# Optimization experiments

Measured on AMD Instinct MI355X. Metric: run time of the kernel, lower is better.

## Reference

```python
import jax, jax.numpy as jnp
import numpy as np

B, T, C, H, DH = 2, 2048, 768, 12, 64


def setup_inputs() -> dict:
    key = jax.random.key(0)
    k1, k2, k3 = jax.random.split(key, 3)
    x = jax.random.normal(k1, (B, T, C), dtype=jnp.float32)
    Wqkv = jax.random.normal(k2, (C, 3 * C), dtype=jnp.float32) * (C ** -0.5)
    Wout = jax.random.normal(k3, (C, C), dtype=jnp.float32) * (C ** -0.5)
    return {"x": x, "Wqkv": Wqkv, "Wout": Wout}


def reference(x, Wqkv, Wout):
    b, t, c = x.shape
    qkv = x @ Wqkv  # [B,T,3C]
    q, k, v = jnp.split(qkv, 3, axis=-1)
    # [B,T,C] -> [B,H,T,dh]
    q = q.reshape(b, t, H, DH).transpose(0, 2, 1, 3)
    k = k.reshape(b, t, H, DH).transpose(0, 2, 1, 3)
    v = v.reshape(b, t, H, DH).transpose(0, 2, 1, 3)
    scale = DH ** -0.5
    scores = jnp.einsum('bhqd,bhkd->bhqk', q, k) * scale  # [B,H,T,T]
    causal = jnp.tril(jnp.ones((t, t), dtype=bool))
    scores = jnp.where(causal, scores, -jnp.inf)
    weights = jax.nn.softmax(scores, axis=-1)
    # dropout p=0.0 -> identity
    out = jnp.einsum('bhqk,bhkd->bhqd', weights, v)  # [B,H,T,dh]
    out = out.transpose(0, 2, 1, 3).reshape(b, t, c)
    return out @ Wout
```

## Files before the change

kernel.cpp:

```cpp
#include <hip/hip_runtime.h>
#include <hip/hip_bf16.h>

#define Bn 2
#define Tn 2048
#define Cn 768
#define Hn 12
#define Dn 64
#define N3n 2304
#define Mn 4096

#define MASKVAL (-30000.f)
#define NITEMS 768
#define DEFER_THR 64.f
#define L2E8 0.1803368801111204f

typedef unsigned short u16;
typedef __attribute__((ext_vector_type(8))) unsigned short ushort8_t;
typedef __attribute__((ext_vector_type(8))) short bf16x8;
typedef __attribute__((ext_vector_type(4))) float f32x4;
typedef __attribute__((address_space(1))) unsigned int* gas1_t;
typedef __attribute__((address_space(3))) unsigned int* las3_t;

__device__ __forceinline__ float bf2f(u16 u) {
  union { unsigned int i; float f; } v; v.i = ((unsigned int)u) << 16; return v.f;
}
__device__ __forceinline__ u16 f2bf(float f) {
  union { float f; unsigned int i; } v; v.f = f;
  return (u16)((v.i + 0x7fffu + ((v.i >> 16) & 1u)) >> 16);
}

__global__ __launch_bounds__(256) void cast_bf16(const float* __restrict__ in,
                                                 u16* __restrict__ out,
                                                 int* __restrict__ counter) {
  if (blockIdx.x == 0 && threadIdx.x == 0) *counter = 0;
  const int i = (blockIdx.x * 256 + threadIdx.x) * 4;
  float4 v = *(const float4*)(in + i);
  ushort4 s;
  s.x = f2bf(v.x); s.y = f2bf(v.y); s.z = f2bf(v.z); s.w = f2bf(v.w);
  *(ushort4*)(out + i) = s;
}

__global__ __launch_bounds__(256) void transpose_cast(const float* __restrict__ in,
                                                      u16* __restrict__ out,
                                                      int R, int Cc) {
  __shared__ u16 t[32][33];
  const int c0 = blockIdx.x * 32, r0 = blockIdx.y * 32;
  const int tx = threadIdx.x, ty = threadIdx.y;
#pragma unroll
  for (int i = 0; i < 4; i++)
    t[ty * 4 + i][tx] = f2bf(in[(size_t)(r0 + ty * 4 + i) * Cc + c0 + tx]);
  __syncthreads();
#pragma unroll
  for (int i = 0; i < 4; i++)
    out[(size_t)(c0 + ty * 4 + i) * R + r0 + tx] = t[tx][ty * 4 + i];
}

#define BK 64

template <int EPI>
__global__ __launch_bounds__(256) void mfma_gemm(const u16* __restrict__ A,
                                                 const u16* __restrict__ BT,
                                                 u16* __restrict__ Q,
                                                 u16* __restrict__ Kd,
                                                 u16* __restrict__ VT,
                                                 float* __restrict__ out) {
  __shared__ __align__(16) u16 Ash[128 * BK];
  __shared__ __align__(16) u16 Bsh[128 * BK];
  const int tid = threadIdx.x;
  const int wv = tid >> 6, lane = tid & 63;
  const int lo = lane & 15, quad = lane >> 4;
  const int wm = wv & 1, wn = wv >> 1;

  const int nwg = gridDim.x * gridDim.y;
  const int cpx = nwg >> 3;
  const int lid = blockIdx.y * gridDim.x + blockIdx.x;
  const int swz = (lid & 7) * cpx + (lid >> 3);
  const int n0 = (swz % gridDim.x) * 128;
  const int m0 = (swz / gridDim.x) * 128;

  const int srow = lane >> 3;
  const int scol = (lane & 7) << 3;

  f32x4 acc[4][4];
#pragma unroll
  for (int i = 0; i < 4; i++)
#pragma unroll
    for (int j = 0; j < 4; j++) acc[i][j] = f32x4{0.f, 0.f, 0.f, 0.f};

  for (int k0 = 0; k0 < Cn; k0 += BK) {
    __syncthreads();
#pragma unroll
    for (int c = 0; c < 4; c++) {
      const int rb = (wv << 5) + (c << 3);
      const int gr = rb + srow;
      __builtin_amdgcn_global_load_lds(
          (gas1_t)(A + (size_t)(m0 + gr) * Cn + k0 + scol),
          (las3_t)(&Ash[rb * BK]), 16, 0, 0);
      __builtin_amdgcn_global_load_lds(
          (gas1_t)(BT + (size_t)(n0 + gr) * Cn + k0 + scol),
          (las3_t)(&Bsh[rb * BK]), 16, 0, 0);
    }
    __syncthreads();

    bf16x8 af[4][2], bfr[4][2];
#pragma unroll
    for (int t = 0; t < 4; t++) {
#pragma unroll
      for (int s = 0; s < 2; s++) {
        af[t][s]  = *(const bf16x8*)&Ash[(wm * 64 + t * 16 + lo) * BK + s * 32 + (quad << 3)];
        bfr[t][s] = *(const bf16x8*)&Bsh[(wn * 64 + t * 16 + lo) * BK + s * 32 + (quad << 3)];
      }
    }
#pragma unroll
    for (int mt = 0; mt < 4; mt++)
#pragma unroll
      for (int nt = 0; nt < 4; nt++) {
        acc[mt][nt] = __builtin_amdgcn_mfma_f32_16x16x32_bf16(af[mt][0], bfr[nt][0],
                                                              acc[mt][nt], 0, 0, 0);
        acc[mt][nt] = __builtin_amdgcn_mfma_f32_16x16x32_bf16(af[mt][1], bfr[nt][1],
                                                              acc[mt][nt], 0, 0, 0);
      }
  }

  if (EPI == 0) {
    const int which = n0 / Cn;
    const int h = ((n0 % Cn) >> 6) + wn;
    const int bb = m0 >> 11;
    const int t_base = (m0 & (Tn - 1)) + wm * 64;
    if (which < 2) {
      u16* dst = ((which == 0) ? Q : Kd) + (size_t)(bb * Hn + h) * Tn * Dn;
#pragma unroll
      for (int mt = 0; mt < 4; mt++)
#pragma unroll
        for (int nt = 0; nt < 4; nt++)
#pragma unroll
          for (int r = 0; r < 4; r++) {
            const int t = t_base + mt * 16 + (quad << 2) + r;
            dst[(size_t)t * Dn + nt * 16 + lo] = f2bf(acc[mt][nt][r]);
          }
    } else {
      u16* dst = VT + (size_t)(bb * Hn + h) * Dn * Tn;
#pragma unroll
      for (int mt = 0; mt < 4; mt++)
#pragma unroll
        for (int nt = 0; nt < 4; nt++) {
          const int t = t_base + mt * 16 + (quad << 2);
          const int d = nt * 16 + lo;
          ushort4 st;
          st.x = f2bf(acc[mt][nt][0]); st.y = f2bf(acc[mt][nt][1]);
          st.z = f2bf(acc[mt][nt][2]); st.w = f2bf(acc[mt][nt][3]);
          *(ushort4*)&dst[(size_t)d * Tn + t] = st;
        }
    }
  } else {
#pragma unroll
    for (int mt = 0; mt < 4; mt++)
#pragma unroll
      for (int nt = 0; nt < 4; nt++)
#pragma unroll
        for (int r = 0; r < 4; r++) {
          const int m = m0 + wm * 64 + mt * 16 + (quad << 2) + r;
          out[(size_t)m * Cn + n0 + wn * 64 + nt * 16 + lo] = acc[mt][nt][r];
        }
  }
}

#define KP 72
#define TILE_W (64 * KP)

__global__ __launch_bounds__(256) void attn_kernel(const u16* __restrict__ Q,
                                                   const u16* __restrict__ K,
                                                   const u16* __restrict__ VT,
                                                   u16* __restrict__ O,
                                                   int* __restrict__ counter) {
  __shared__ __align__(16) u16 Ksh[2 * TILE_W];
  __shared__ __align__(16) u16 Vsh[2 * TILE_W];
  __shared__ __align__(16) u16 Pw[4][16 * KP];
  __shared__ int s_item;

  const int tid = threadIdx.x;
  const int wv = tid >> 6, lane = tid & 63;
  const int lo = lane & 15, quad = lane >> 4;
  const int sr = tid >> 3;
  const int sc = (tid & 7) << 3;

  for (;;) {
    if (tid == 0) s_item = atomicAdd(counter, 1);
    __syncthreads();
    const int item = s_item;
    if (item >= NITEMS) return;

    const int q0 = (31 - item / 24) * 64;
    const int hb = item % 24;
    const int h = hb % 12, b = hb / 12;
    const size_t base = (size_t)(b * Hn + h) * Tn * Dn;
    const size_t vtb  = (size_t)(b * Hn + h) * Dn * Tn;

    const u16* qp = Q + base + (size_t)(q0 + (wv << 4) + lo) * Dn + (quad << 3);
    const bf16x8 aq0 = *(const bf16x8*)qp;
    const bf16x8 aq1 = *(const bf16x8*)(qp + 32);

    f32x4 o[4] = {f32x4{0,0,0,0}, f32x4{0,0,0,0}, f32x4{0,0,0,0}, f32x4{0,0,0,0}};
    float m1 = MASKVAL;
    float l1 = 0.f;

#pragma unroll
    for (int it = 0; it < 2; it++) {
      const int r = sr + it * 32;
      *(ushort8_t*)&Ksh[r * KP + sc] =
          *(const ushort8_t*)(K + base + (size_t)r * Dn + sc);
      *(ushort8_t*)&Vsh[r * KP + sc] =
          *(const ushort8_t*)(VT + vtb + (size_t)r * Tn + sc);
    }
    __syncthreads();

    int cur = 0;
    const int qrel = (wv << 4) + lo;

    for (int j0 = 0; j0 <= q0; j0 += 64) {
      const bool hasnext = (j0 + 64 <= q0);

      ushort8_t kr[2], vr[2];
      if (hasnext) {
#pragma unroll
        for (int it = 0; it < 2; it++) {
          const int r = sr + it * 32;
          kr[it] = *(const ushort8_t*)(K + base + (size_t)(j0 + 64 + r) * Dn + sc);
          vr[it] = *(const ushort8_t*)(VT + vtb + (size_t)r * Tn + j0 + 64 + sc);
        }
      }

      const u16* Kb_ = &Ksh[cur * TILE_W];
      const u16* Vb_ = &Vsh[cur * TILE_W];

      f32x4 s[4];
      __builtin_amdgcn_s_setprio(1);
#pragma unroll
      for (int nt = 0; nt < 4; nt++) {
        const bf16x8 bk0 = *(const bf16x8*)(&Kb_[(nt * 16 + lo) * KP + (quad << 3)]);
        const bf16x8 bk1 = *(const bf16x8*)(&Kb_[(nt * 16 + lo) * KP + 32 + (quad << 3)]);
        f32x4 a = {0.f, 0.f, 0.f, 0.f};
        a = __builtin_amdgcn_mfma_f32_16x16x32_bf16(bk0, aq0, a, 0, 0, 0);
        a = __builtin_amdgcn_mfma_f32_16x16x32_bf16(bk1, aq1, a, 0, 0, 0);
        s[nt] = a;
      }
      __builtin_amdgcn_s_setprio(0);

      if (j0 == q0) {
#pragma unroll
        for (int nt = 0; nt < 4; nt++)
#pragma unroll
          for (int r = 0; r < 4; r++) {
            const int kv = nt * 16 + (quad << 2) + r;
            if (kv > qrel) s[nt][r] = MASKVAL;
          }
      }

      float mx = fmaxf(s[0][0], s[0][1]);
      mx = fmaxf(fmaxf(mx, s[0][2]), s[0][3]);
      mx = fmaxf(fmaxf(mx, s[1][0]), s[1][1]);
      mx = fmaxf(fmaxf(mx, s[1][2]), s[1][3]);
      mx = fmaxf(fmaxf(mx, s[2][0]), s[2][1]);
      mx = fmaxf(fmaxf(mx, s[2][2]), s[2][3]);
      mx = fmaxf(fmaxf(mx, s[3][0]), s[3][1]);
      mx = fmaxf(fmaxf(mx, s[3][2]), s[3][3]);
      const float pmax = mx;

      if (!__all(pmax <= m1 + DEFER_THR)) {
        float mr = fmaxf(pmax, __shfl_xor(pmax, 16));
        mr = fmaxf(mr, __shfl_xor(mr, 32));
        const float mnew = fmaxf(m1, mr);
        const float alpha = __builtin_amdgcn_exp2f(L2E8 * (m1 - mnew));
        m1 = mnew;
        l1 *= alpha;
        float ar[4];
#pragma unroll
        for (int r = 0; r < 4; r++) ar[r] = __shfl(alpha, (quad << 2) + r);
#pragma unroll
        for (int nt = 0; nt < 4; nt++)
#pragma unroll
          for (int r = 0; r < 4; r++) o[nt][r] *= ar[r];
      }

      const float mb2 = L2E8 * m1;
      float sum = 0.f;
#pragma unroll
      for (int nt = 0; nt < 4; nt++)
#pragma unroll
        for (int r = 0; r < 4; r++) {
          const float p = __builtin_amdgcn_exp2f(L2E8 * s[nt][r] - mb2);
          s[nt][r] = p;
          sum += p;
        }
      l1 += sum;

      u16* pw = Pw[wv];
#pragma unroll
      for (int nt = 0; nt < 4; nt++) {
        unsigned int p01, p23;
        asm("v_cvt_pk_bf16_f32 %0, %1, %2" : "=v"(p01) : "v"(s[nt][0]), "v"(s[nt][1]));
        asm("v_cvt_pk_bf16_f32 %0, %1, %2" : "=v"(p23) : "v"(s[nt][2]), "v"(s[nt][3]));
        *(uint2*)&pw[lo * KP + nt * 16 + (quad << 2)] = make_uint2(p01, p23);
      }
      const bf16x8 pa0 = *(const bf16x8*)(&pw[lo * KP + (quad << 3)]);
      const bf16x8 pa1 = *(const bf16x8*)(&pw[lo * KP + 32 + (quad << 3)]);

      __builtin_amdgcn_s_setprio(1);
#pragma unroll
      for (int nt = 0; nt < 4; nt++) {
        const bf16x8 bv0 = *(const bf16x8*)(&Vb_[(nt * 16 + lo) * KP + (quad << 3)]);
        const bf16x8 bv1 = *(const bf16x8*)(&Vb_[(nt * 16 + lo) * KP + 32 + (quad << 3)]);
        o[nt] = __builtin_amdgcn_mfma_f32_16x16x32_bf16(pa0, bv0, o[nt], 0, 0, 0);
        o[nt] = __builtin_amdgcn_mfma_f32_16x16x32_bf16(pa1, bv1, o[nt], 0, 0, 0);
      }
      __builtin_amdgcn_s_setprio(0);

      if (hasnext) {
        const int nb = cur ^ 1;
#pragma unroll
        for (int it = 0; it < 2; it++) {
          const int r = sr + it * 32;
          *(ushort8_t*)&Ksh[nb * TILE_W + r * KP + sc] = kr[it];
          *(ushort8_t*)&Vsh[nb * TILE_W + r * KP + sc] = vr[it];
        }
      }
      __syncthreads();
      cur ^= 1;
    }

    float lt = l1;
    lt += __shfl_xor(lt, 16);
    lt += __shfl_xor(lt, 32);
    const float linv = 1.f / lt;
    float ir[4];
#pragma unroll
    for (int r = 0; r < 4; r++) ir[r] = __shfl(linv, (quad << 2) + r);
#pragma unroll
    for (int nt = 0; nt < 4; nt++)
#pragma unroll
      for (int r = 0; r < 4; r++) {
        const int row = q0 + (wv << 4) + (quad << 2) + r;
        const int col = h * 64 + nt * 16 + lo;
        O[(size_t)(b * Tn + row) * Cn + col] = f2bf(o[nt][r] * ir[r]);
      }
  }
}

extern "C" void kernel_launch(void* const* d_in, const int* in_sizes, int n_in,
                              void* d_out, int out_size, void* d_ws, size_t ws_size,
                              hipStream_t stream) {
  const float* x    = (const float*)d_in[0];
  const float* Wqkv = (const float*)d_in[1];
  const float* Wout = (const float*)d_in[2];
  float* out = (float*)d_out;

  const size_t per = (size_t)Bn * Hn * Tn * Dn;
  u16* xb    = (u16*)d_ws;
  u16* WqkvT = xb + (size_t)Mn * Cn;
  u16* WoutT = WqkvT + (size_t)N3n * Cn;
  u16* Qb    = WoutT + (size_t)Cn * Cn;
  u16* Kb    = Qb + per;
  u16* VTb   = Kb + per;
  u16* attn  = VTb + per;
  int* counter = (int*)(attn + (size_t)Mn * Cn);

  cast_bf16<<<(Mn * Cn) / 1024, 256, 0, stream>>>(x, xb, counter);
  transpose_cast<<<dim3(N3n / 32, Cn / 32), dim3(32, 8), 0, stream>>>(Wqkv, WqkvT, Cn, N3n);
  transpose_cast<<<dim3(Cn / 32, Cn / 32), dim3(32, 8), 0, stream>>>(Wout, WoutT, Cn, Cn);

  mfma_gemm<0><<<dim3(N3n / 128, Mn / 128), 256, 0, stream>>>(xb, WqkvT, Qb, Kb, VTb, nullptr);
  attn_kernel<<<dim3(640), 256, 0, stream>>>(Qb, Kb, VTb, attn, counter);
  mfma_gemm<1><<<dim3(Cn / 128, Mn / 128), 256, 0, stream>>>(attn, WoutT, nullptr, nullptr, nullptr, out);
}
```

Before: 181.2 us.

## Split long causal attention query tiles into KV chunks with combine pass

Query tiles 16-31 have their causal KV range split into two chunks, and a constant schedule table orders work items longest-first. Each split chunk writes an fp32 partial output with its row max and sum, and a new combine kernel merges the two halves. The goal is to remove the load imbalance from long causal rows and keep the whole GPU busy, at the cost of an extra launch and partial-buffer traffic. The two weight transpose launches are merged into one, and the setprio hints and inline bf16 pack asm are dropped.

```diff
diff --git a/kernel.cpp b/kernel.cpp
--- a/kernel.cpp
+++ b/kernel.cpp
@@ -10,7 +10,7 @@
 #define Mn 4096
 
 #define MASKVAL (-30000.f)
-#define NITEMS 768
+#define NITEMS 1152
 #define DEFER_THR 64.f
 #define L2E8 0.1803368801111204f
 
@@ -28,6 +28,20 @@
   union { float f; unsigned int i; } v; v.f = f;
   return (u16)((v.i + 0x7fffu + ((v.i >> 16) & 1u)) >> 16);
 }
+
+#define E(qt, s0, s1, ck) (((qt) << 24) | ((s0) << 16) | ((s1) << 8) | (ck))
+__constant__ unsigned int SCHED[48] = {
+    E(31, 0, 16, 0), E(31, 16, 32, 1), E(30, 0, 16, 0), E(15, 0, 16, 2),
+    E(30, 16, 31, 1), E(29, 0, 15, 0), E(29, 15, 30, 1), E(28, 0, 15, 0), E(14, 0, 15, 2),
+    E(28, 15, 29, 1), E(27, 0, 14, 0), E(27, 14, 28, 1), E(26, 0, 14, 0), E(13, 0, 14, 2),
+    E(26, 14, 27, 1), E(25, 0, 13, 0), E(25, 13, 26, 1), E(24, 0, 13, 0), E(12, 0, 13, 2),
+    E(24, 13, 25, 1), E(23, 0, 12, 0), E(23, 12, 24, 1), E(22, 0, 12, 0), E(11, 0, 12, 2),
+    E(22, 12, 23, 1), E(21, 0, 11, 0), E(21, 11, 22, 1), E(20, 0, 11, 0), E(10, 0, 11, 2),
+    E(20, 11, 21, 1), E(19, 0, 10, 0), E(19, 10, 20, 1), E(18, 0, 10, 0), E(9, 0, 10, 2),
+    E(18, 10, 19, 1), E(17, 0, 9, 0), E(17, 9, 18, 1), E(16, 0, 9, 0), E(8, 0, 9, 2),
+    E(16, 9, 17, 1), E(7, 0, 8, 2),
+    E(6, 0, 7, 2), E(5, 0, 6, 2), E(4, 0, 5, 2), E(3, 0, 4, 2), E(2, 0, 3, 2),
+    E(1, 0, 2, 2), E(0, 0, 1, 2)};
 
 __global__ __launch_bounds__(256) void cast_bf16(const float* __restrict__ in,
                                                  u16* __restrict__ out,
@@ -40,11 +54,17 @@
   *(ushort4*)(out + i) = s;
 }
 
-__global__ __launch_bounds__(256) void transpose_cast(const float* __restrict__ in,
-                                                      u16* __restrict__ out,
-                                                      int R, int Cc) {
+__global__ __launch_bounds__(256) void transpose_cast_w(const float* __restrict__ Wqkv,
+                                                        const float* __restrict__ Wout,
+                                                        u16* __restrict__ WqkvT,
+                                                        u16* __restrict__ WoutT) {
   __shared__ u16 t[32][33];
-  const int c0 = blockIdx.x * 32, r0 = blockIdx.y * 32;
+  const bool isA = blockIdx.x < (N3n / 32);
+  const float* in = isA ? Wqkv : Wout;
+  u16* out = isA ? WqkvT : WoutT;
+  const int Cc = isA ? N3n : Cn;
+  const int c0 = (isA ? blockIdx.x : blockIdx.x - N3n / 32) * 32;
+  const int r0 = blockIdx.y * 32;
   const int tx = threadIdx.x, ty = threadIdx.y;
 #pragma unroll
   for (int i = 0; i < 4; i++)
@@ -52,7 +72,7 @@
   __syncthreads();
 #pragma unroll
   for (int i = 0; i < 4; i++)
-    out[(size_t)(c0 + ty * 4 + i) * R + r0 + tx] = t[tx][ty * 4 + i];
+    out[(size_t)(c0 + ty * 4 + i) * Cn + r0 + tx] = t[tx][ty * 4 + i];
 }
 
 #define BK 64
@@ -172,7 +192,10 @@
                                                    const u16* __restrict__ K,
                                                    const u16* __restrict__ VT,
                                                    u16* __restrict__ O,
-                                                   int* __restrict__ counter) {
+                                                   int* __restrict__ counter,
+                                                   float* __restrict__ po,
+                                                   float* __restrict__ pm,
+                                                   float* __restrict__ pl) {
   __shared__ __align__(16) u16 Ksh[2 * TILE_W];
   __shared__ __align__(16) u16 Vsh[2 * TILE_W];
   __shared__ __align__(16) u16 Pw[4][16 * KP];
@@ -190,7 +213,11 @@
     const int item = s_item;
     if (item >= NITEMS) return;
 
-    const int q0 = (31 - item / 24) * 64;
+    const unsigned int e = SCHED[item / 24];
+    const int qt = e >> 24, ck = e & 255;
+    const int jstart = ((e >> 16) & 255) << 6;
+    const int jend   = ((e >> 8) & 255) << 6;
+    const int q0 = qt << 6;
     const int hb = item % 24;
     const int h = hb % 12, b = hb / 12;
     const size_t base = (size_t)(b * Hn + h) * Tn * Dn;
@@ -208,17 +235,17 @@
     for (int it = 0; it < 2; it++) {
       const int r = sr + it * 32;
       *(ushort8_t*)&Ksh[r * KP + sc] =
-          *(const ushort8_t*)(K + base + (size_t)r * Dn + sc);
+          *(const ushort8_t*)(K + base + (size_t)(jstart + r) * Dn + sc);
       *(ushort8_t*)&Vsh[r * KP + sc] =
-          *(const ushort8_t*)(VT + vtb + (size_t)r * Tn + sc);
+          *(const ushort8_t*)(VT + vtb + (size_t)r * Tn + jstart + sc);
     }
     __syncthreads();
 
     int cur = 0;
     const int qrel = (wv << 4) + lo;
 
-    for (int j0 = 0; j0 <= q0; j0 += 64) {
-      const bool hasnext = (j0 + 64 <= q0);
+    for (int j0 = jstart; j0 < jend; j0 += 64) {
+      const bool hasnext = (j0 + 64 < jend);
 
       ushort8_t kr[2], vr[2];
       if (hasnext) {
@@ -234,7 +261,6 @@
       const u16* Vb_ = &Vsh[cur * TILE_W];
 
       f32x4 s[4];
-      __builtin_amdgcn_s_setprio(1);
 #pragma unroll
       for (int nt = 0; nt < 4; nt++) {
         const bf16x8 bk0 = *(const bf16x8*)(&Kb_[(nt * 16 + lo) * KP + (quad << 3)]);
@@ -244,7 +270,6 @@
         a = __builtin_amdgcn_mfma_f32_16x16x32_bf16(bk1, aq1, a, 0, 0, 0);
         s[nt] = a;
       }
-      __builtin_amdgcn_s_setprio(0);
 
       if (j0 == q0) {
 #pragma unroll
@@ -297,15 +322,14 @@
       u16* pw = Pw[wv];
 #pragma unroll
       for (int nt = 0; nt < 4; nt++) {
-        unsigned int p01, p23;
-        asm("v_cvt_pk_bf16_f32 %0, %1, %2" : "=v"(p01) : "v"(s[nt][0]), "v"(s[nt][1]));
-        asm("v_cvt_pk_bf16_f32 %0, %1, %2" : "=v"(p23) : "v"(s[nt][2]), "v"(s[nt][3]));
-        *(uint2*)&pw[lo * KP + nt * 16 + (quad << 2)] = make_uint2(p01, p23);
+        ushort4 pk;
+        pk.x = f2bf(s[nt][0]); pk.y = f2bf(s[nt][1]);
+        pk.z = f2bf(s[nt][2]); pk.w = f2bf(s[nt][3]);
+        *(ushort4*)&pw[lo * KP + nt * 16 + (quad << 2)] = pk;
       }
       const bf16x8 pa0 = *(const bf16x8*)(&pw[lo * KP + (quad << 3)]);
       const bf16x8 pa1 = *(const bf16x8*)(&pw[lo * KP + 32 + (quad << 3)]);
 
-      __builtin_amdgcn_s_setprio(1);
 #pragma unroll
       for (int nt = 0; nt < 4; nt++) {
         const bf16x8 bv0 = *(const bf16x8*)(&Vb_[(nt * 16 + lo) * KP + (quad << 3)]);
@@ -313,7 +337,6 @@
         o[nt] = __builtin_amdgcn_mfma_f32_16x16x32_bf16(pa0, bv0, o[nt], 0, 0, 0);
         o[nt] = __builtin_amdgcn_mfma_f32_16x16x32_bf16(pa1, bv1, o[nt], 0, 0, 0);
       }
-      __builtin_amdgcn_s_setprio(0);
 
       if (hasnext) {
         const int nb = cur ^ 1;
@@ -335,14 +358,63 @@
     float ir[4];
 #pragma unroll
     for (int r = 0; r < 4; r++) ir[r] = __shfl(linv, (quad << 2) + r);
-#pragma unroll
-    for (int nt = 0; nt < 4; nt++)
-#pragma unroll
-      for (int r = 0; r < 4; r++) {
-        const int row = q0 + (wv << 4) + (quad << 2) + r;
-        const int col = h * 64 + nt * 16 + lo;
-        O[(size_t)(b * Tn + row) * Cn + col] = f2bf(o[nt][r] * ir[r]);
-      }
+
+    if (ck == 2) {
+#pragma unroll
+      for (int nt = 0; nt < 4; nt++)
+#pragma unroll
+        for (int r = 0; r < 4; r++) {
+          const int row = q0 + (wv << 4) + (quad << 2) + r;
+          const int col = h * 64 + nt * 16 + lo;
+          O[(size_t)(b * Tn + row) * Cn + col] = f2bf(o[nt][r] * ir[r]);
+        }
+    } else {
+      const int st = hb * 16 + (qt - 16);
+      const int pidx = st * 2 + ck;
+      float* pO = po + ((size_t)pidx << 12);
+#pragma unroll
+      for (int nt = 0; nt < 4; nt++)
+#pragma unroll
+        for (int r = 0; r < 4; r++)
+          pO[((wv << 4) + (quad << 2) + r) * 64 + nt * 16 + lo] = o[nt][r] * ir[r];
+      if (quad == 0) {
+        pm[pidx * 64 + (wv << 4) + lo] = m1;
+        pl[pidx * 64 + (wv << 4) + lo] = lt;
+      }
+    }
+  }
+}
+
+__global__ __launch_bounds__(256) void combine_kernel(const float* __restrict__ po,
+                                                      const float* __restrict__ pm,
+                                                      const float* __restrict__ pl,
+                                                      u16* __restrict__ O) {
+  const int st = blockIdx.x;
+  const int hb = st >> 4;
+  const int h = hb % 12, b = hb / 12;
+  const int q0 = (16 + (st & 15)) << 6;
+  const int tid = threadIdx.x;
+  const int row = tid >> 2, cc0 = (tid & 3) << 4;
+  const float* pa = po + (((size_t)st * 2) << 12) + row * 64 + cc0;
+  const float* pb = pa + 4096;
+  const float ma = pm[st * 128 + row],      la = pl[st * 128 + row];
+  const float mb = pm[st * 128 + 64 + row], lb = pl[st * 128 + 64 + row];
+  const float mm = fmaxf(ma, mb);
+  float wa = la * __builtin_amdgcn_exp2f(L2E8 * (ma - mm));
+  float wb = lb * __builtin_amdgcn_exp2f(L2E8 * (mb - mm));
+  const float wi = 1.f / (wa + wb);
+  wa *= wi; wb *= wi;
+  u16* Orow = O + (size_t)(b * Tn + q0 + row) * Cn + h * 64 + cc0;
+#pragma unroll
+  for (int i = 0; i < 16; i += 4) {
+    const float4 va = *(const float4*)(pa + i);
+    const float4 vb = *(const float4*)(pb + i);
+    ushort4 s4;
+    s4.x = f2bf(wa * va.x + wb * vb.x);
+    s4.y = f2bf(wa * va.y + wb * vb.y);
+    s4.z = f2bf(wa * va.z + wb * vb.z);
+    s4.w = f2bf(wa * va.w + wb * vb.w);
+    *(ushort4*)(Orow + i) = s4;
   }
 }
 
@@ -363,12 +435,16 @@
   u16* VTb   = Kb + per;
   u16* attn  = VTb + per;
   int* counter = (int*)(attn + (size_t)Mn * Cn);
+  float* po = (float*)(counter + 512);
+  float* pm = po + (size_t)768 * 4096;
+  float* pl = pm + (size_t)768 * 64;
 
   cast_bf16<<<(Mn * Cn) / 1024, 256, 0, stream>>>(x, xb, counter);
-  transpose_cast<<<dim3(N3n / 32, Cn / 32), dim3(32, 8), 0, stream>>>(Wqkv, WqkvT, Cn, N3n);
-  transpose_cast<<<dim3(Cn / 32, Cn / 32), dim3(32, 8), 0, stream>>>(Wout, WoutT, Cn, Cn);
+  transpose_cast_w<<<dim3(N3n / 32 + Cn / 32, Cn / 32), dim3(32, 8), 0, stream>>>(
+      Wqkv, Wout, WqkvT, WoutT);
 
   mfma_gemm<0><<<dim3(N3n / 128, Mn / 128), 256, 0, stream>>>(xb, WqkvT, Qb, Kb, VTb, nullptr);
-  attn_kernel<<<dim3(640), 256, 0, stream>>>(Qb, Kb, VTb, attn, counter);
+  attn_kernel<<<dim3(768), 256, 0, stream>>>(Qb, Kb, VTb, attn, counter, po, pm, pl);
+  combine_kernel<<<dim3(384), 256, 0, stream>>>(po, pm, pl, attn);
   mfma_gemm<1><<<dim3(Cn / 128, Mn / 128), 256, 0, stream>>>(attn, WoutT, nullptr, nullptr, nullptr, out);
 }
```

After: 184.9 us. 1.02x slower.
